# Kernel tuning notes

Measured on AMD Instinct MI355X. Metric: run time of the kernel, lower is better.

## Reference

```python
import jax, jax.numpy as jnp
import numpy as np

N, E, G = 65536, 524288, 1024
ND, ED, HID, H, C = 21, 12, 128, 4, 32
L = 8  # num_blocks * 2 conv layers
EPS = 1e-5


def _gatv2(x, src, dst, ea, Wl, Wr, We, att, bias):
    # PyG GATv2Conv: xl=lin_l(x) (source), xr=lin_r(x) (target)
    n = x.shape[0]
    xl = jnp.einsum('nd,dhc->nhc', x, Wl)   # [N,H,C]
    xr = jnp.einsum('nd,dhc->nhc', x, Wr)
    el = jnp.einsum('ed,dhc->ehc', ea, We)  # [E,H,C]
    m = xl[src] + xr[dst] + el              # per-edge message pre-activation
    e = jnp.einsum('ehc,hc->eh', jax.nn.leaky_relu(m, 0.2), att)  # [E,H]
    # scatter softmax over incoming edges of each dst node
    emax = jax.ops.segment_max(e, dst, num_segments=n)
    emax = jnp.where(jnp.isfinite(emax), emax, 0.0)
    p = jnp.exp(e - emax[dst])
    denom = jax.ops.segment_sum(p, dst, num_segments=n)
    alpha = p / jnp.clip(denom, 1e-16)[dst]
    out = jax.ops.segment_sum(alpha[..., None] * xl[src], dst, num_segments=n)
    return out.reshape(n, H * C) + bias


def _bn(x, scale, bias):
    mu = x.mean(0)
    var = x.var(0)
    return (x - mu) * jax.lax.rsqrt(var + EPS) * scale + bias


def setup_inputs():
    key = jax.random.key(0)
    ks = jax.random.split(key, 16)
    f = lambda k, shp, s=0.05: jax.random.normal(k, shp, jnp.float32) * s
    return dict(
        x=f(ks[0], (N, ND), 1.0),
        edge_attr=f(ks[1], (E, ED), 1.0),
        edge_index=jax.random.randint(ks[2], (2, E), 0, N),
        batch=jnp.sort(jax.random.randint(ks[3], (N,), 0, G)),
        Win=f(ks[4], (ND, HID)), bin_=jnp.zeros(HID),
        Wl=f(ks[5], (L, HID, H, C)), Wr=f(ks[6], (L, HID, H, C)),
        We=f(ks[7], (L, ED, H, C)), att=f(ks[8], (L, H, C)),
        bconv=jnp.zeros((L, HID)),
        bn_scale=jnp.ones((L, HID)), bn_bias=jnp.zeros((L, HID)),
        Wv1=f(ks[9], (HID, 64)), bv1=jnp.zeros(64),
        Wv2=f(ks[10], (64, 3)), bv2=jnp.zeros(3),
        Wp1=f(ks[11], (2 * HID + ED, 64)), bp1=jnp.zeros(64),
        Wp2=f(ks[12], (64, 1)), bp2=jnp.zeros(1),
    )


def reference(x, edge_attr, edge_index, batch, Win, bin_, Wl, Wr, We, att,
              bconv, bn_scale, bn_bias, Wv1, bv1, Wv2, bv2, Wp1, bp1, Wp2, bp2):
    src0, dst0 = edge_index[0], edge_index[1]
    # add_self_loops with fill_value='mean' for edge features
    ones_e = jnp.ones((E,), x.dtype)
    deg = jax.ops.segment_sum(ones_e, dst0, num_segments=N)
    mean_ea = jax.ops.segment_sum(edge_attr, dst0, num_segments=N) / jnp.clip(deg, 1.0)[:, None]
    ar = jnp.arange(N)
    src = jnp.concatenate([src0, ar])
    dst = jnp.concatenate([dst0, ar])
    ea = jnp.concatenate([edge_attr, mean_ea], axis=0)

    h = jax.nn.relu(x @ Win + bin_)
    for b in range(L // 2):
        i, j = 2 * b, 2 * b + 1
        res = h
        h = _gatv2(h, src, dst, ea, Wl[i], Wr[i], We[i], att[i], bconv[i])
        h = jax.nn.relu(_bn(h, bn_scale[i], bn_bias[i]))
        h = _gatv2(h, src, dst, ea, Wl[j], Wr[j], We[j], att[j], bconv[j])
        h = _bn(h, bn_scale[j], bn_bias[j])
        h = jax.nn.relu(h + res)

    counts = jax.ops.segment_sum(jnp.ones((N,), h.dtype), batch, num_segments=G)
    pooled = jax.ops.segment_sum(h, batch, num_segments=G) / jnp.clip(counts, 1.0)[:, None]
    value_logits = jax.nn.relu(pooled @ Wv1 + bv1) @ Wv2 + bv2  # [G,3]

    edge_input = jnp.concatenate([h[src0], h[dst0], edge_attr], axis=1)  # [E, 2*HID+ED]
    policy_logits = (jax.nn.relu(edge_input @ Wp1 + bp1) @ Wp2 + bp2)[:, 0]  # [E]
    return value_logits, policy_logits
```

## Files before the change

### kernel.cpp

```cpp
#include <hip/hip_runtime.h>
#include <hip/hip_fp16.h>

#define NN 65536
#define EE 524288
#define EPX 589824
#define GG 1024
#define NSLOT 16

typedef __attribute__((ext_vector_type(8))) short bf16x8;
typedef __attribute__((ext_vector_type(4))) float f32x4;

#define LOG2E 1.44269504088896f


__device__ __forceinline__ unsigned short f2bf(float x) {
    unsigned int u = __float_as_uint(x);
    u += 0x7FFFu + ((u >> 16) & 1u);
    return (unsigned short)(u >> 16);
}
__device__ __forceinline__ float bflo(unsigned int w) { return __uint_as_float(w << 16); }
__device__ __forceinline__ float bfhi(unsigned int w) { return __uint_as_float(w & 0xFFFF0000u); }
__device__ __forceinline__ float lrelu(float x) { return fmaf(0.4f, fabsf(x), 0.6f * x); }
__device__ __forceinline__ unsigned int packh2(float a, float b) {
    __half2 h = __floats2half2_rn(a, b);
    return *reinterpret_cast<unsigned int*>(&h);
}


__launch_bounds__(256)
__global__ void k_deg(const int* __restrict__ dst0, int* __restrict__ deg)
{
    int e = blockIdx.x * 256 + threadIdx.x;
    if (e >= EE) return;
    atomicAdd(&deg[dst0[e]], 1);
}

__launch_bounds__(1024)
__global__ void k_scan(const int* __restrict__ deg, int* __restrict__ rowptr)
{
    __shared__ int sums[1024];
    int t = threadIdx.x;
    int base = t * 64;
    int s = 0;
    for (int i = 0; i < 64; i++) s += deg[base + i] + 1;
    sums[t] = s;
    __syncthreads();
    for (int off = 1; off < 1024; off <<= 1) {
        int v = (t >= off) ? sums[t - off] : 0;
        __syncthreads();
        sums[t] += v;
        __syncthreads();
    }
    int off = sums[t] - s;
    for (int i = 0; i < 64; i++) { rowptr[base + i] = off; off += deg[base + i] + 1; }
    if (t == 1023) rowptr[NN] = off;
}

__launch_bounds__(256)
__global__ void k_scatter(const int* __restrict__ src0, const int* __restrict__ dst0,
                          const float* __restrict__ eattr,
                          const int* __restrict__ rowptr, const int* __restrict__ deg,
                          int* __restrict__ fill, int* __restrict__ csr_src,
                          unsigned short* __restrict__ eaCSR)
{
    int e = blockIdx.x * 256 + threadIdx.x;
    if (e >= EPX) return;
    if (e < EE) {
        int d = dst0[e];
        int pos = rowptr[d] + atomicAdd(&fill[d], 1);
        csr_src[pos] = src0[e] << 8;
        const float* ep = eattr + (size_t)e * 12;
        float4 a = *reinterpret_cast<const float4*>(ep);
        float4 b = *reinterpret_cast<const float4*>(ep + 4);
        float4 c = *reinterpret_cast<const float4*>(ep + 8);
        uint2* q = reinterpret_cast<uint2*>(eaCSR + (size_t)pos * 12);
        q[0] = make_uint2(packh2(a.x, a.y), packh2(a.z, a.w));
        q[1] = make_uint2(packh2(b.x, b.y), packh2(b.z, b.w));
        q[2] = make_uint2(packh2(c.x, c.y), packh2(c.z, c.w));
    } else {
        int n = e - EE;
        csr_src[rowptr[n] + deg[n]] = n << 8;
    }
}

__launch_bounds__(256)
__global__ void k_selfattr(const int* __restrict__ rowptr, unsigned short* __restrict__ eaCSR)
{
    int tid = blockIdx.x * 256 + threadIdx.x;
    int n = tid >> 4;
    int lk = tid & 15;
    if (lk >= 12) return;
    int beg = rowptr[n], endm1 = rowptr[n + 1] - 1;
    float s = 0.f;
    for (int p = beg; p < endm1; ++p) {
        __half h = *reinterpret_cast<const __half*>(&eaCSR[(size_t)p * 12 + lk]);
        s += __half2float(h);
    }
    float dv = fmaxf((float)(endm1 - beg), 1.0f);
    __half ho = __float2half(s / dv);
    eaCSR[(size_t)endm1 * 12 + lk] = *reinterpret_cast<unsigned short*>(&ho);
}


__launch_bounds__(256)
__global__ void k_wprep(const float* __restrict__ Wl, const float* __restrict__ Wr,
                        const float* __restrict__ Wp1,
                        unsigned short* __restrict__ wg, unsigned short* __restrict__ wp)
{
    int tid = blockIdx.x * 256 + threadIdx.x;
    if (tid < 32768) {
        int l = tid >> 12;
        int r = tid & 4095;
        int kt = r >> 10, ct = (r >> 6) & 15, lane = r & 63;
        int kb = kt * 32 + (lane >> 4) * 8;
        int col = ct * 16 + (lane & 15);
        const float* W = (col < 128) ? (Wl + (size_t)l * 16384 + col)
                                     : (Wr + (size_t)l * 16384 + (col - 128));
        unsigned short* o = wg + (size_t)tid * 8;
#pragma unroll
        for (int j = 0; j < 8; j++) o[j] = f2bf(W[(size_t)(kb + j) * 128]);
    } else if (tid < 34816) {
        int r = tid - 32768;
        int kt = r >> 9, ct = (r >> 6) & 7, lane = r & 63;
        int kb = kt * 32 + (lane >> 4) * 8;
        int col = ct * 16 + (lane & 15);
        const float* W = (col < 64) ? (Wp1 + col) : (Wp1 + 128 * 64 + (col - 64));
        unsigned short* o = wp + (size_t)r * 8;
#pragma unroll
        for (int j = 0; j < 8; j++) o[j] = f2bf(W[(size_t)(kb + j) * 64]);
    }
}


__launch_bounds__(256)
__global__ void k_input(const float* __restrict__ x, const float* __restrict__ Win,
                        const float* __restrict__ bin, float* __restrict__ h)
{
    __shared__ float W[21 * 128];
    int t = threadIdx.x;
    for (int i = t; i < 21 * 128; i += 256) W[i] = Win[i];
    __syncthreads();
    int c = t & 127, sub = t >> 7;
    int n0 = blockIdx.x * 16;
    float bc = bin[c];
    for (int i = 0; i < 8; i++) {
        int n = n0 + sub + i * 2;
        const float* xp = x + (size_t)n * 21;
        float acc = bc;
#pragma unroll
        for (int k = 0; k < 21; k++) acc = fmaf(xp[k], W[k * 128 + c], acc);
        h[(size_t)n * 128 + c] = fmaxf(acc, 0.f);
    }
}


__device__ __forceinline__ void load_afrag(const float* __restrict__ A, int arow, int kb,
                                           bf16x8 af[4])
{
#pragma unroll
    for (int kt = 0; kt < 4; kt++) {
        const float* ap = A + (size_t)arow * 128 + kt * 32 + kb;
        float4 lo = *reinterpret_cast<const float4*>(ap);
        float4 hi = *reinterpret_cast<const float4*>(ap + 4);
        bf16x8 v;
        v[0] = (short)f2bf(lo.x); v[1] = (short)f2bf(lo.y);
        v[2] = (short)f2bf(lo.z); v[3] = (short)f2bf(lo.w);
        v[4] = (short)f2bf(hi.x); v[5] = (short)f2bf(hi.y);
        v[6] = (short)f2bf(hi.z); v[7] = (short)f2bf(hi.w);
        af[kt] = v;
    }
}

__device__ __forceinline__ void gemm_gat_core(const bf16x8 af[4], const unsigned short* __restrict__ Bf,
                                              int row0, unsigned short* __restrict__ Cl,
                                              unsigned short* __restrict__ Cr, int lane)
{
    int crow = row0 + (lane >> 4) * 4;
    int c0 = lane & 15;
#pragma unroll
    for (int ct = 0; ct < 16; ct++) {
        f32x4 acc = {0.f, 0.f, 0.f, 0.f};
#pragma unroll
        for (int kt = 0; kt < 4; kt++) {
            bf16x8 bf = *reinterpret_cast<const bf16x8*>(Bf + ((size_t)(kt * 16 + ct) * 64 + lane) * 8);
            acc = __builtin_amdgcn_mfma_f32_16x16x32_bf16(af[kt], bf, acc, 0, 0, 0);
        }
        int col = ct * 16 + c0;
        unsigned short* C = (col < 128) ? Cl : Cr;
        int cc = col & 127;
#pragma unroll
        for (int r = 0; r < 4; r++)
            C[(size_t)(crow + r) * 128 + cc] = f2bf(acc[r]);
    }
}

__launch_bounds__(256)
__global__ void k_gemm_gat(const float* __restrict__ A, const unsigned short* __restrict__ Bf,
                           unsigned short* __restrict__ Cl, unsigned short* __restrict__ Cr)
{
    int wave = threadIdx.x >> 6, lane = threadIdx.x & 63;
    int row0 = blockIdx.x * 64 + wave * 16;
    bf16x8 af[4];
    load_afrag(A, row0 + (lane & 15), (lane >> 4) * 8, af);
    gemm_gat_core(af, Bf, row0, Cl, Cr, lane);
}

__launch_bounds__(256)
__global__ void k_gemm_gat_bn(const float* __restrict__ G, const float* __restrict__ bnstat,
                              const float* __restrict__ scale, const float* __restrict__ bias,
                              const unsigned short* __restrict__ Bf,
                              unsigned short* __restrict__ Cl, unsigned short* __restrict__ Cr)
{
    __shared__ float sA[128], bA[128];
    int t = threadIdx.x;
    if (t < 128) {
        float sum = 0.f, sq = 0.f;
#pragma unroll
        for (int sl = 0; sl < NSLOT; sl++) {
            sum += bnstat[sl * 256 + t];
            sq  += bnstat[sl * 256 + 128 + t];
        }
        const float invN = 1.0f / (float)NN;
        float mean = sum * invN;
        float var  = sq * invN - mean * mean;
        float sc   = scale[t] * rsqrtf(var + 1e-5f);
        sA[t] = sc;
        bA[t] = bias[t] - mean * sc;
    }
    __syncthreads();
    int wave = t >> 6, lane = t & 63;
    int row0 = blockIdx.x * 64 + wave * 16;
    int arow = row0 + (lane & 15);
    int kb = (lane >> 4) * 8;
    bf16x8 af[4];
#pragma unroll
    for (int kt = 0; kt < 4; kt++) {
        int cb = kt * 32 + kb;
        const float* gp = G + (size_t)arow * 128 + cb;
        float4 lo = *reinterpret_cast<const float4*>(gp);
        float4 hi = *reinterpret_cast<const float4*>(gp + 4);
        bf16x8 v;
        v[0] = (short)f2bf(fmaxf(fmaf(lo.x, sA[cb + 0], bA[cb + 0]), 0.f));
        v[1] = (short)f2bf(fmaxf(fmaf(lo.y, sA[cb + 1], bA[cb + 1]), 0.f));
        v[2] = (short)f2bf(fmaxf(fmaf(lo.z, sA[cb + 2], bA[cb + 2]), 0.f));
        v[3] = (short)f2bf(fmaxf(fmaf(lo.w, sA[cb + 3], bA[cb + 3]), 0.f));
        v[4] = (short)f2bf(fmaxf(fmaf(hi.x, sA[cb + 4], bA[cb + 4]), 0.f));
        v[5] = (short)f2bf(fmaxf(fmaf(hi.y, sA[cb + 5], bA[cb + 5]), 0.f));
        v[6] = (short)f2bf(fmaxf(fmaf(hi.z, sA[cb + 6], bA[cb + 6]), 0.f));
        v[7] = (short)f2bf(fmaxf(fmaf(hi.w, sA[cb + 7], bA[cb + 7]), 0.f));
        af[kt] = v;
    }
    gemm_gat_core(af, Bf, row0, Cl, Cr, lane);
}

__launch_bounds__(256)
__global__ void k_gemm_pol(const float* __restrict__ A, const unsigned short* __restrict__ Bf,
                           float* __restrict__ P)
{
    int wave = threadIdx.x >> 6, lane = threadIdx.x & 63;
    int row0 = blockIdx.x * 64 + wave * 16;
    bf16x8 af[4];
    load_afrag(A, row0 + (lane & 15), (lane >> 4) * 8, af);
    int crow = row0 + (lane >> 4) * 4;
    int c0 = lane & 15;
#pragma unroll
    for (int ct = 0; ct < 8; ct++) {
        f32x4 acc = {0.f, 0.f, 0.f, 0.f};
#pragma unroll
        for (int kt = 0; kt < 4; kt++) {
            bf16x8 bf = *reinterpret_cast<const bf16x8*>(Bf + ((size_t)(kt * 8 + ct) * 64 + lane) * 8);
            acc = __builtin_amdgcn_mfma_f32_16x16x32_bf16(af[kt], bf, acc, 0, 0, 0);
        }
        int col = ct * 16 + c0;
#pragma unroll
        for (int r = 0; r < 4; r++)
            P[(size_t)(crow + r) * 128 + col] = acc[r];
    }
}


__device__ __forceinline__ float2 edge_el(uint2 qa, uint2 qb, uint2 qc,
                                          const __half2 wx[6], const __half2 wy[6])
{
    __half2 e0 = *reinterpret_cast<const __half2*>(&qa.x);
    __half2 e1 = *reinterpret_cast<const __half2*>(&qa.y);
    __half2 e2 = *reinterpret_cast<const __half2*>(&qb.x);
    __half2 e3 = *reinterpret_cast<const __half2*>(&qb.y);
    __half2 e4 = *reinterpret_cast<const __half2*>(&qc.x);
    __half2 e5 = *reinterpret_cast<const __half2*>(&qc.y);
    __half2 ax = __hmul2(e0, wx[0]);
    ax = __hfma2(e1, wx[1], ax); ax = __hfma2(e2, wx[2], ax);
    ax = __hfma2(e3, wx[3], ax); ax = __hfma2(e4, wx[4], ax);
    ax = __hfma2(e5, wx[5], ax);
    __half2 ay = __hmul2(e0, wy[0]);
    ay = __hfma2(e1, wy[1], ay); ay = __hfma2(e2, wy[2], ay);
    ay = __hfma2(e3, wy[3], ay); ay = __hfma2(e4, wy[4], ay);
    ay = __hfma2(e5, wy[5], ay);
    float2 r;
    r.x = __low2float(ax) + __high2float(ax);
    r.y = __low2float(ay) + __high2float(ay);
    return r;
}

__launch_bounds__(256)
__global__ void k_gat(const unsigned short* __restrict__ xlb, const unsigned short* __restrict__ xrb,
                      const unsigned short* __restrict__ eaCSR,
                      const int* __restrict__ rowptr, const int* __restrict__ csr_src,
                      const float* __restrict__ We, const float* __restrict__ att,
                      const float* __restrict__ bconv, float* __restrict__ g,
                      float* __restrict__ bnstat)
{
    int wid = blockIdx.x * 4 + (threadIdx.x >> 6);
    int lane = threadIdx.x & 63;
    int f0 = lane * 2;

    __half2 wx[6], wy[6];
#pragma unroll
    for (int j = 0; j < 6; j++) {
        float2 w0 = *reinterpret_cast<const float2*>(We + (2 * j) * 128 + f0);
        float2 w1 = *reinterpret_cast<const float2*>(We + (2 * j + 1) * 128 + f0);
        wx[j] = __floats2half2_rn(w0.x, w1.x);
        wy[j] = __floats2half2_rn(w0.y, w1.y);
    }
    float2 av = *reinterpret_cast<const float2*>(att + f0);
    av.x *= LOG2E; av.y *= LOG2E;
    float2 bc = *reinterpret_cast<const float2*>(bconv + f0);
    const char* xl_lane = reinterpret_cast<const char*>(xlb) + (lane << 2);

    float bs0 = 0.f, bs1 = 0.f, bq0 = 0.f, bq1 = 0.f;

    for (int n = wid * 8; n < wid * 8 + 8; ++n) {
        unsigned int xrw = *reinterpret_cast<const unsigned int*>(xrb + (size_t)n * 128 + f0);
        float xr0 = bflo(xrw), xr1 = bfhi(xrw);

        float m = -INFINITY, s = 0.f, a0 = 0.f, a1 = 0.f;
        int beg = rowptr[n], end = rowptr[n + 1];
        int idx = beg;
        for (; idx + 2 <= end; idx += 2) {
            int off0 = csr_src[idx], off1 = csr_src[idx + 1];
            const uint2* q0 = reinterpret_cast<const uint2*>(eaCSR + (size_t)idx * 12);
            uint2 qa = q0[0], qb = q0[1], qc = q0[2];
            uint2 ra = q0[3], rb = q0[4], rc = q0[5];
            unsigned int xw0 = *reinterpret_cast<const unsigned int*>(xl_lane + off0);
            unsigned int xw1 = *reinterpret_cast<const unsigned int*>(xl_lane + off1);

            float2 el0 = edge_el(qa, qb, qc, wx, wy);
            float2 el1 = edge_el(ra, rb, rc, wx, wy);

            float xa0 = bflo(xw0), xa1 = bfhi(xw0);
            float xb0 = bflo(xw1), xb1 = bfhi(xw1);

            float t0 = lrelu(xa0 + xr0 + el0.x) * av.x + lrelu(xa1 + xr1 + el0.y) * av.y;
            float t1 = lrelu(xb0 + xr0 + el1.x) * av.x + lrelu(xb1 + xr1 + el1.y) * av.y;
            t0 += __shfl_xor(t0, 1);  t1 += __shfl_xor(t1, 1);
            t0 += __shfl_xor(t0, 2);  t1 += __shfl_xor(t1, 2);
            t0 += __shfl_xor(t0, 4);  t1 += __shfl_xor(t1, 4);
            t0 += __shfl_xor(t0, 8);  t1 += __shfl_xor(t1, 8);

            float nm = fmaxf(m, fmaxf(t0, t1));
            float so = exp2f(m - nm);
            float w0 = exp2f(t0 - nm);
            float w1 = exp2f(t1 - nm);
            s  = fmaf(s, so, w0 + w1);
            a0 = fmaf(a0, so, fmaf(w0, xa0, w1 * xb0));
            a1 = fmaf(a1, so, fmaf(w0, xa1, w1 * xb1));
            m = nm;
        }
        if (idx < end) {
            int off0 = csr_src[idx];
            const uint2* q0 = reinterpret_cast<const uint2*>(eaCSR + (size_t)idx * 12);
            uint2 qa = q0[0], qb = q0[1], qc = q0[2];
            unsigned int xw0 = *reinterpret_cast<const unsigned int*>(xl_lane + off0);
            float2 el0 = edge_el(qa, qb, qc, wx, wy);
            float xa0 = bflo(xw0), xa1 = bfhi(xw0);
            float tt = lrelu(xa0 + xr0 + el0.x) * av.x + lrelu(xa1 + xr1 + el0.y) * av.y;
            tt += __shfl_xor(tt, 1);
            tt += __shfl_xor(tt, 2);
            tt += __shfl_xor(tt, 4);
            tt += __shfl_xor(tt, 8);
            float nm = fmaxf(m, tt);
            float so = exp2f(m - nm);
            float w  = exp2f(tt - nm);
            s  = fmaf(s, so, w);
            a0 = fmaf(a0, so, w * xa0);
            a1 = fmaf(a1, so, w * xa1);
            m = nm;
        }
        float inv = 1.f / s;
        float r0 = fmaf(a0, inv, bc.x);
        float r1 = fmaf(a1, inv, bc.y);
        *reinterpret_cast<float2*>(g + (size_t)n * 128 + f0) = make_float2(r0, r1);
        bs0 += r0; bs1 += r1;
        bq0 = fmaf(r0, r0, bq0); bq1 = fmaf(r1, r1, bq1);
    }

    __shared__ float red[256 * 4];
    int t = threadIdx.x;
    red[t * 4 + 0] = bs0; red[t * 4 + 1] = bs1;
    red[t * 4 + 2] = bq0; red[t * 4 + 3] = bq1;
    __syncthreads();
    if (t < 64) {
        float v0 = red[t * 4 + 0] + red[(t + 64) * 4 + 0] + red[(t + 128) * 4 + 0] + red[(t + 192) * 4 + 0];
        float v1 = red[t * 4 + 1] + red[(t + 64) * 4 + 1] + red[(t + 128) * 4 + 1] + red[(t + 192) * 4 + 1];
        float q0 = red[t * 4 + 2] + red[(t + 64) * 4 + 2] + red[(t + 128) * 4 + 2] + red[(t + 192) * 4 + 2];
        float q1 = red[t * 4 + 3] + red[(t + 64) * 4 + 3] + red[(t + 128) * 4 + 3] + red[(t + 192) * 4 + 3];
        float* slot = bnstat + (size_t)(blockIdx.x & (NSLOT - 1)) * 256;
        atomicAdd(&slot[2 * t + 0], v0);
        atomicAdd(&slot[2 * t + 1], v1);
        atomicAdd(&slot[128 + 2 * t + 0], q0);
        atomicAdd(&slot[128 + 2 * t + 1], q1);
    }
}


__launch_bounds__(256)
__global__ void k_bnapply_res_relu(const float4* __restrict__ gin,
                                   const float* __restrict__ bnstat,
                                   const float* __restrict__ scale, const float* __restrict__ bias,
                                   float4* __restrict__ hbuf)
{
    __shared__ float sA[128], bA[128];
    int t = threadIdx.x;
    if (t < 128) {
        float sum = 0.f, sq = 0.f;
#pragma unroll
        for (int sl = 0; sl < NSLOT; sl++) {
            sum += bnstat[sl * 256 + t];
            sq  += bnstat[sl * 256 + 128 + t];
        }
        const float invN = 1.0f / (float)NN;
        float mean = sum * invN;
        float var  = sq * invN - mean * mean;
        float sc   = scale[t] * rsqrtf(var + 1e-5f);
        sA[t] = sc;
        bA[t] = bias[t] - mean * sc;
    }
    __syncthreads();
    int idx = blockIdx.x * 256 + t;
    int c4 = (idx & 31) * 4;
    float4 v = gin[idx];
    float4 hv = hbuf[idx];
    float4 r;
    r.x = fmaxf(fmaf(v.x, sA[c4 + 0], bA[c4 + 0]) + hv.x, 0.f);
    r.y = fmaxf(fmaf(v.y, sA[c4 + 1], bA[c4 + 1]) + hv.y, 0.f);
    r.z = fmaxf(fmaf(v.z, sA[c4 + 2], bA[c4 + 2]) + hv.z, 0.f);
    r.w = fmaxf(fmaf(v.w, sA[c4 + 3], bA[c4 + 3]) + hv.w, 0.f);
    hbuf[idx] = r;
}


__launch_bounds__(128)
__global__ void k_pool(const float* __restrict__ h, const int* __restrict__ batch,
                       float* __restrict__ pooled, float* __restrict__ cnt)
{
    int c = threadIdx.x;
    int r0 = blockIdx.x * 128;
    int cur = batch[r0];
    float acc = 0.f;
    float run = 0.f;
    for (int i = 0; i < 128; ++i) {
        int r = r0 + i;
        int b = batch[r];
        if (b != cur) {
            atomicAdd(&pooled[(size_t)cur * 128 + c], acc);
            if (c == 0) atomicAdd(&cnt[cur], run);
            acc = 0.f; run = 0.f; cur = b;
        }
        acc += h[(size_t)r * 128 + c];
        run += 1.f;
    }
    atomicAdd(&pooled[(size_t)cur * 128 + c], acc);
    if (c == 0) atomicAdd(&cnt[cur], run);
}

__launch_bounds__(64)
__global__ void k_value(const float* __restrict__ pooled, const float* __restrict__ cnt,
                        const float* __restrict__ Wv1, const float* __restrict__ bv1,
                        const float* __restrict__ Wv2, const float* __restrict__ bv2,
                        float* __restrict__ out)
{
    int gi = blockIdx.x;
    int l = threadIdx.x;
    float inv = 1.f / fmaxf(cnt[gi], 1.f);
    const float* pr = pooled + (size_t)gi * 128;
    float z = bv1[l];
    for (int k = 0; k < 128; k++) z = fmaf(pr[k] * inv, Wv1[k * 64 + l], z);
    z = fmaxf(z, 0.f);
#pragma unroll
    for (int j = 0; j < 3; j++) {
        float p = z * Wv2[l * 3 + j];
        p += __shfl_xor(p, 32); p += __shfl_xor(p, 16); p += __shfl_xor(p, 8);
        p += __shfl_xor(p, 4);  p += __shfl_xor(p, 2);  p += __shfl_xor(p, 1);
        if (l == 0) out[gi * 3 + j] = p + bv2[j];
    }
}


__launch_bounds__(256)
__global__ void k_policy(const float* __restrict__ P,
                         const float* __restrict__ eattr,
                         const int* __restrict__ src0, const int* __restrict__ dst0,
                         const float* __restrict__ Wp1c, const float* __restrict__ bp1,
                         const float* __restrict__ Wp2, const float* __restrict__ bp2,
                         float* __restrict__ out)
{
    int wave = (blockIdx.x * 256 + threadIdx.x) >> 6;
    int lane = threadIdx.x & 63;
    float w1c[12];
#pragma unroll
    for (int k = 0; k < 12; k++) w1c[k] = Wp1c[k * 64 + lane];
    float wp2 = Wp2[lane];
    float bb = bp1[lane];
    float b2 = bp2[0];
    for (int i = 0; i < 8; i++) {
        int e = wave * 8 + i;
        int sI = src0[e], dI = dst0[e];
        const float* ep = eattr + (size_t)e * 12;
        float4 e0 = *reinterpret_cast<const float4*>(ep);
        float4 e1 = *reinterpret_cast<const float4*>(ep + 4);
        float4 e2 = *reinterpret_cast<const float4*>(ep + 8);
        float z = P[(size_t)sI * 128 + lane] + P[(size_t)dI * 128 + 64 + lane] + bb;
        z += e0.x * w1c[0] + e0.y * w1c[1] + e0.z * w1c[2]  + e0.w * w1c[3]
           + e1.x * w1c[4] + e1.y * w1c[5] + e1.z * w1c[6]  + e1.w * w1c[7]
           + e2.x * w1c[8] + e2.y * w1c[9] + e2.z * w1c[10] + e2.w * w1c[11];
        z = fmaxf(z, 0.f);
        float p = z * wp2;
        p += __shfl_xor(p, 32); p += __shfl_xor(p, 16); p += __shfl_xor(p, 8);
        p += __shfl_xor(p, 4);  p += __shfl_xor(p, 2);  p += __shfl_xor(p, 1);
        if (lane == 0) out[3072 + e] = p + b2;
    }
}


extern "C" void kernel_launch(void* const* d_in, const int* in_sizes, int n_in,
                              void* d_out, int out_size, void* d_ws, size_t ws_size,
                              hipStream_t stream)
{
    const float* x     = (const float*)d_in[0];
    const float* eattr = (const float*)d_in[1];
    const int*   eidx  = (const int*)d_in[2];
    const int*   batch = (const int*)d_in[3];
    const float* Win   = (const float*)d_in[4];
    const float* bin   = (const float*)d_in[5];
    const float* Wl    = (const float*)d_in[6];
    const float* Wr    = (const float*)d_in[7];
    const float* We    = (const float*)d_in[8];
    const float* att   = (const float*)d_in[9];
    const float* bconv = (const float*)d_in[10];
    const float* bnsc  = (const float*)d_in[11];
    const float* bnbi  = (const float*)d_in[12];
    const float* Wv1   = (const float*)d_in[13];
    const float* bv1   = (const float*)d_in[14];
    const float* Wv2   = (const float*)d_in[15];
    const float* bv2   = (const float*)d_in[16];
    const float* Wp1   = (const float*)d_in[17];
    const float* bp1   = (const float*)d_in[18];
    const float* Wp2   = (const float*)d_in[19];
    const float* bp2   = (const float*)d_in[20];
    float* out = (float*)d_out;

    const int* src0 = eidx;
    const int* dst0 = eidx + EE;

    const size_t NH = (size_t)NN * 128;
    float* ws = (float*)d_ws;
    float* h  = ws;
    float* g  = h + NH;
    unsigned short* xlb = (unsigned short*)(g + NH);
    unsigned short* xrb = xlb + NH;
    unsigned short* eaCSR = xrb + NH;
    int* rowptr = (int*)(eaCSR + (size_t)EPX * 12);
    int* csr_src = rowptr + (NN + 1);
    int* deg  = csr_src + EPX;
    int* fill = deg + NN;
    float* bnstat = (float*)(fill + NN);
    float* pooled = bnstat + 8 * NSLOT * 256;
    float* cnt    = pooled + (size_t)GG * 128;
    size_t zero_elems = (size_t)NN + NN + 8 * NSLOT * 256 + (size_t)GG * 128 + GG;
    unsigned short* wg = (unsigned short*)(cnt + GG);
    unsigned short* wp = wg + 8 * 32768;

    hipMemsetAsync(deg, 0, zero_elems * sizeof(float), stream);

    k_deg<<<EE / 256, 256, 0, stream>>>(dst0, deg);
    k_scan<<<1, 1024, 0, stream>>>(deg, rowptr);
    k_scatter<<<EPX / 256, 256, 0, stream>>>(src0, dst0, eattr, rowptr, deg, fill, csr_src, eaCSR);
    k_selfattr<<<(NN * 16) / 256, 256, 0, stream>>>(rowptr, eaCSR);
    k_wprep<<<136, 256, 0, stream>>>(Wl, Wr, Wp1, wg, wp);

    k_input<<<NN / 16, 256, 0, stream>>>(x, Win, bin, h);

    for (int l = 0; l < 8; l++) {
        float* bs = bnstat + (size_t)l * NSLOT * 256;
        if (l % 2 == 0) {
            k_gemm_gat<<<NN / 64, 256, 0, stream>>>(h, wg + (size_t)l * 32768, xlb, xrb);
        } else {
            float* bsp = bnstat + (size_t)(l - 1) * NSLOT * 256;
            k_gemm_gat_bn<<<NN / 64, 256, 0, stream>>>(g, bsp,
                                                       bnsc + (size_t)(l - 1) * 128,
                                                       bnbi + (size_t)(l - 1) * 128,
                                                       wg + (size_t)l * 32768, xlb, xrb);
        }
        k_gat<<<NN / 32, 256, 0, stream>>>(xlb, xrb, eaCSR, rowptr, csr_src,
                                           We + (size_t)l * 1536, att + (size_t)l * 128,
                                           bconv + (size_t)l * 128, g, bs);
        if (l % 2 == 1) {
            k_bnapply_res_relu<<<(NN * 128 / 4) / 256, 256, 0, stream>>>(
                (const float4*)g, bs, bnsc + (size_t)l * 128, bnbi + (size_t)l * 128,
                (float4*)h);
        }
    }

    k_pool<<<NN / 128, 128, 0, stream>>>(h, batch, pooled, cnt);
    k_value<<<GG, 64, 0, stream>>>(pooled, cnt, Wv1, bv1, Wv2, bv2, out);

    float* P = g;
    k_gemm_pol<<<NN / 64, 256, 0, stream>>>(h, wp, P);
    k_policy<<<NN / 4, 256, 0, stream>>>(P, eattr, src0, dst0,
                                         Wp1 + 256 * 64, bp1, Wp2, bp2, out);
}
```

Baseline: 1.202 ms.

## Unroll GAT edge loop by four, halve nodes per wave, store policy projections in bf16

The GAT aggregation loop now processes four incoming edges per iteration instead of two, which exposes more independent gathers and shuffle reductions to hide memory latency. Each wave handles four nodes instead of eight, with twice the blocks launched and twice the BN-stat slots. The policy head's per-node projection P is written in bf16 into the xlb buffer, halving the bytes gathered per edge in k_policy. In exchange, the policy logits carry bf16 rounding error and the wider unroll uses more registers.

```diff
diff --git a/kernel.cpp b/kernel.cpp
--- a/kernel.cpp
+++ b/kernel.cpp
@@ -5,7 +5,7 @@
 #define EE 524288
 #define EPX 589824
 #define GG 1024
-#define NSLOT 16
+#define NSLOT 32
 
 typedef __attribute__((ext_vector_type(8))) short bf16x8;
 typedef __attribute__((ext_vector_type(4))) float f32x4;
@@ -20,6 +20,7 @@
 }
 __device__ __forceinline__ float bflo(unsigned int w) { return __uint_as_float(w << 16); }
 __device__ __forceinline__ float bfhi(unsigned int w) { return __uint_as_float(w & 0xFFFF0000u); }
+__device__ __forceinline__ float bf2f(unsigned short u) { return __uint_as_float((unsigned int)u << 16); }
 __device__ __forceinline__ float lrelu(float x) { return fmaf(0.4f, fabsf(x), 0.6f * x); }
 __device__ __forceinline__ unsigned int packh2(float a, float b) {
     __half2 h = __floats2half2_rn(a, b);
@@ -255,7 +256,7 @@
 
 __launch_bounds__(256)
 __global__ void k_gemm_pol(const float* __restrict__ A, const unsigned short* __restrict__ Bf,
-                           float* __restrict__ P)
+                           unsigned short* __restrict__ P)
 {
     int wave = threadIdx.x >> 6, lane = threadIdx.x & 63;
     int row0 = blockIdx.x * 64 + wave * 16;
@@ -274,7 +275,7 @@
         int col = ct * 16 + c0;
 #pragma unroll
         for (int r = 0; r < 4; r++)
-            P[(size_t)(crow + r) * 128 + col] = acc[r];
+            P[(size_t)(crow + r) * 128 + col] = f2bf(acc[r]);
     }
 }
 
@@ -302,6 +303,15 @@
     return r;
 }
 
+__device__ __forceinline__ float head_reduce(float t)
+{
+    t += __shfl_xor(t, 1);
+    t += __shfl_xor(t, 2);
+    t += __shfl_xor(t, 4);
+    t += __shfl_xor(t, 8);
+    return t;
+}
+
 __launch_bounds__(256)
 __global__ void k_gat(const unsigned short* __restrict__ xlb, const unsigned short* __restrict__ xrb,
                       const unsigned short* __restrict__ eaCSR,
@@ -329,55 +339,63 @@
 
     float bs0 = 0.f, bs1 = 0.f, bq0 = 0.f, bq1 = 0.f;
 
-    for (int n = wid * 8; n < wid * 8 + 8; ++n) {
+    for (int n = wid * 4; n < wid * 4 + 4; ++n) {
         unsigned int xrw = *reinterpret_cast<const unsigned int*>(xrb + (size_t)n * 128 + f0);
         float xr0 = bflo(xrw), xr1 = bfhi(xrw);
 
         float m = -INFINITY, s = 0.f, a0 = 0.f, a1 = 0.f;
         int beg = rowptr[n], end = rowptr[n + 1];
         int idx = beg;
-        for (; idx + 2 <= end; idx += 2) {
-            int off0 = csr_src[idx], off1 = csr_src[idx + 1];
-            const uint2* q0 = reinterpret_cast<const uint2*>(eaCSR + (size_t)idx * 12);
-            uint2 qa = q0[0], qb = q0[1], qc = q0[2];
-            uint2 ra = q0[3], rb = q0[4], rc = q0[5];
+        for (; idx + 4 <= end; idx += 4) {
+            int off0 = csr_src[idx],     off1 = csr_src[idx + 1];
+            int off2 = csr_src[idx + 2], off3 = csr_src[idx + 3];
+            const uint2* q = reinterpret_cast<const uint2*>(eaCSR + (size_t)idx * 12);
+            uint2 qa = q[0], qb = q[1],  qc = q[2];
+            uint2 ra = q[3], rb = q[4],  rc = q[5];
+            uint2 sa = q[6], sb = q[7],  sc = q[8];
+            uint2 ta = q[9], tb = q[10], tc = q[11];
             unsigned int xw0 = *reinterpret_cast<const unsigned int*>(xl_lane + off0);
             unsigned int xw1 = *reinterpret_cast<const unsigned int*>(xl_lane + off1);
+            unsigned int xw2 = *reinterpret_cast<const unsigned int*>(xl_lane + off2);
+            unsigned int xw3 = *reinterpret_cast<const unsigned int*>(xl_lane + off3);
 
             float2 el0 = edge_el(qa, qb, qc, wx, wy);
             float2 el1 = edge_el(ra, rb, rc, wx, wy);
+            float2 el2 = edge_el(sa, sb, sc, wx, wy);
+            float2 el3 = edge_el(ta, tb, tc, wx, wy);
 
             float xa0 = bflo(xw0), xa1 = bfhi(xw0);
             float xb0 = bflo(xw1), xb1 = bfhi(xw1);
+            float xc0 = bflo(xw2), xc1 = bfhi(xw2);
+            float xd0 = bflo(xw3), xd1 = bfhi(xw3);
 
             float t0 = lrelu(xa0 + xr0 + el0.x) * av.x + lrelu(xa1 + xr1 + el0.y) * av.y;
             float t1 = lrelu(xb0 + xr0 + el1.x) * av.x + lrelu(xb1 + xr1 + el1.y) * av.y;
-            t0 += __shfl_xor(t0, 1);  t1 += __shfl_xor(t1, 1);
-            t0 += __shfl_xor(t0, 2);  t1 += __shfl_xor(t1, 2);
-            t0 += __shfl_xor(t0, 4);  t1 += __shfl_xor(t1, 4);
-            t0 += __shfl_xor(t0, 8);  t1 += __shfl_xor(t1, 8);
-
-            float nm = fmaxf(m, fmaxf(t0, t1));
+            float t2 = lrelu(xc0 + xr0 + el2.x) * av.x + lrelu(xc1 + xr1 + el2.y) * av.y;
+            float t3 = lrelu(xd0 + xr0 + el3.x) * av.x + lrelu(xd1 + xr1 + el3.y) * av.y;
+            t0 = head_reduce(t0); t1 = head_reduce(t1);
+            t2 = head_reduce(t2); t3 = head_reduce(t3);
+
+            float nm = fmaxf(fmaxf(fmaxf(t0, t1), fmaxf(t2, t3)), m);
             float so = exp2f(m - nm);
             float w0 = exp2f(t0 - nm);
             float w1 = exp2f(t1 - nm);
-            s  = fmaf(s, so, w0 + w1);
-            a0 = fmaf(a0, so, fmaf(w0, xa0, w1 * xb0));
-            a1 = fmaf(a1, so, fmaf(w0, xa1, w1 * xb1));
+            float w2 = exp2f(t2 - nm);
+            float w3 = exp2f(t3 - nm);
+            s  = fmaf(s, so, (w0 + w1) + (w2 + w3));
+            a0 = fmaf(a0, so, fmaf(w0, xa0, fmaf(w1, xb0, fmaf(w2, xc0, w3 * xd0))));
+            a1 = fmaf(a1, so, fmaf(w0, xa1, fmaf(w1, xb1, fmaf(w2, xc1, w3 * xd1))));
             m = nm;
         }
-        if (idx < end) {
+        for (; idx < end; ++idx) {
             int off0 = csr_src[idx];
-            const uint2* q0 = reinterpret_cast<const uint2*>(eaCSR + (size_t)idx * 12);
-            uint2 qa = q0[0], qb = q0[1], qc = q0[2];
+            const uint2* q = reinterpret_cast<const uint2*>(eaCSR + (size_t)idx * 12);
+            uint2 qa = q[0], qb = q[1], qc = q[2];
             unsigned int xw0 = *reinterpret_cast<const unsigned int*>(xl_lane + off0);
             float2 el0 = edge_el(qa, qb, qc, wx, wy);
             float xa0 = bflo(xw0), xa1 = bfhi(xw0);
             float tt = lrelu(xa0 + xr0 + el0.x) * av.x + lrelu(xa1 + xr1 + el0.y) * av.y;
-            tt += __shfl_xor(tt, 1);
-            tt += __shfl_xor(tt, 2);
-            tt += __shfl_xor(tt, 4);
-            tt += __shfl_xor(tt, 8);
+            tt = head_reduce(tt);
             float nm = fmaxf(m, tt);
             float so = exp2f(m - nm);
             float w  = exp2f(tt - nm);
@@ -497,7 +515,7 @@
 
 
 __launch_bounds__(256)
-__global__ void k_policy(const float* __restrict__ P,
+__global__ void k_policy(const unsigned short* __restrict__ P,
                          const float* __restrict__ eattr,
                          const int* __restrict__ src0, const int* __restrict__ dst0,
                          const float* __restrict__ Wp1c, const float* __restrict__ bp1,
@@ -519,7 +537,7 @@
         float4 e0 = *reinterpret_cast<const float4*>(ep);
         float4 e1 = *reinterpret_cast<const float4*>(ep + 4);
         float4 e2 = *reinterpret_cast<const float4*>(ep + 8);
-        float z = P[(size_t)sI * 128 + lane] + P[(size_t)dI * 128 + 64 + lane] + bb;
+        float z = bf2f(P[(size_t)sI * 128 + lane]) + bf2f(P[(size_t)dI * 128 + 64 + lane]) + bb;
         z += e0.x * w1c[0] + e0.y * w1c[1] + e0.z * w1c[2]  + e0.w * w1c[3]
            + e1.x * w1c[4] + e1.y * w1c[5] + e1.z * w1c[6]  + e1.w * w1c[7]
            + e2.x * w1c[8] + e2.y * w1c[9] + e2.z * w1c[10] + e2.w * w1c[11];
@@ -601,7 +619,7 @@
                                                        bnbi + (size_t)(l - 1) * 128,
                                                        wg + (size_t)l * 32768, xlb, xrb);
         }
-        k_gat<<<NN / 32, 256, 0, stream>>>(xlb, xrb, eaCSR, rowptr, csr_src,
+        k_gat<<<NN / 16, 256, 0, stream>>>(xlb, xrb, eaCSR, rowptr, csr_src,
                                            We + (size_t)l * 1536, att + (size_t)l * 128,
                                            bconv + (size_t)l * 128, g, bs);
         if (l % 2 == 1) {
@@ -614,7 +632,7 @@
     k_pool<<<NN / 128, 128, 0, stream>>>(h, batch, pooled, cnt);
     k_value<<<GG, 64, 0, stream>>>(pooled, cnt, Wv1, bv1, Wv2, bv2, out);
 
-    float* P = g;
+    unsigned short* P = xlb;
     k_gemm_pol<<<NN / 64, 256, 0, stream>>>(h, wp, P);
     k_policy<<<NN / 4, 256, 0, stream>>>(P, eattr, src0, dst0,
                                          Wp1 + 256 * 64, bp1, Wp2, bp2, out);
```

After: 1.133 ms. -5.7%, faster.
